# Performance work log

Hardware: AMD Instinct MI355X
Metric: run time of the kernel (lower is better)

## Reference

```python
import jax, jax.numpy as jnp
from jax import lax
import numpy as np

B, CIN, COUT, N, H, W = 16, 64, 64, 8, 128, 128


def setup_inputs() -> dict:
    key = jax.random.key(0)
    ks = jax.random.split(key, 6)
    s = 0.05
    return {
        "x": jax.random.normal(ks[0], (B, CIN, H, W), dtype=jnp.float32),
        "condition": jax.random.normal(ks[1], (B, CIN), dtype=jnp.float32),
        "filt_w": jax.random.normal(ks[2], (N, COUT, CIN, 3, 3), dtype=jnp.float32) * s,
        "filt_b": jax.random.normal(ks[3], (N, COUT), dtype=jnp.float32) * s,
        "sel_w": jax.random.normal(ks[4], (N, CIN), dtype=jnp.float32) * s,
        "sel_b": jax.random.normal(ks[5], (N,), dtype=jnp.float32) * s,
    }


def reference(x, condition, filt_w, filt_b, sel_w, sel_b):
    b = x.shape[0]
    # condition selector: Linear(in_channels -> num_conditions) + softmax
    logits = condition.reshape(b, -1) @ sel_w.T + sel_b          # [B, N]
    weights = jax.nn.softmax(logits, axis=-1)                    # [B, N]

    n, cout, cin, kh, kw = filt_w.shape
    # Run all N branch convs in ONE conv by stacking filters on the output-channel axis.
    kern = filt_w.reshape(n * cout, cin, kh, kw)
    y = lax.conv_general_dilated(
        x, kern, window_strides=(1, 1), padding="SAME",
        dimension_numbers=("NCHW", "OIHW", "NCHW"))              # [B, N*COUT, H, W]
    h, w = y.shape[-2], y.shape[-1]
    y = y.reshape(b, n, cout, h, w) + filt_b.reshape(1, n, cout, 1, 1)
    # softmax-gated sum over the N branches
    out = jnp.einsum("bn,bnohw->bohw", weights, y)
    return out
```

## Files before the change

### kernel.cpp

```cpp
#include <hip/hip_runtime.h>
#include <stdint.h>

#define BATCH 16
#define CIN   64
#define COUT  64
#define NBR   8
#define HH    128
#define WW    128


typedef __attribute__((ext_vector_type(8)))  short short8;
typedef __attribute__((ext_vector_type(16))) float f32x16;

__device__ __forceinline__ unsigned short f2bf(float f) {
    union { float f; uint32_t u; } v; v.f = f;
    uint32_t u = v.u;
    return (unsigned short)((u + 0x7FFFu + ((u >> 16) & 1u)) >> 16);
}

__global__ void k_weights(const float* __restrict__ cond,
                          const float* __restrict__ sel_w,
                          const float* __restrict__ sel_b,
                          float* __restrict__ wt) {
    __shared__ float lg[BATCH][NBR];
    int t = threadIdx.x;
    int b = t >> 3, n = t & 7;
    float acc = sel_b[n];
    #pragma unroll
    for (int c = 0; c < CIN; ++c)
        acc += cond[b * CIN + c] * sel_w[n * CIN + c];
    lg[b][n] = acc;
    __syncthreads();
    float m = -1e30f;
    #pragma unroll
    for (int i = 0; i < NBR; ++i) m = fmaxf(m, lg[b][i]);
    float s = 0.f;
    #pragma unroll
    for (int i = 0; i < NBR; ++i) s += __expf(lg[b][i] - m);
    wt[t] = __expf(lg[b][n] - m) / s;
}

__global__ void k_combine(const float* __restrict__ filt_w,
                          const float* __restrict__ filt_b,
                          const float* __restrict__ wt,
                          unsigned short* __restrict__ wfilt,
                          float* __restrict__ cbias) {
    const int NF = BATCH * 9 * COUT * CIN;
    int idx = blockIdx.x * 256 + threadIdx.x;
    if (idx < NF) {
        int c  = idx & 63;
        int o  = (idx >> 6) & 63;
        int bt = idx >> 12;
        int t  = bt % 9;
        int b  = bt / 9;
        float acc = 0.f;
        #pragma unroll
        for (int n = 0; n < NBR; ++n)
            acc += wt[b * NBR + n] * filt_w[((n * COUT + o) * CIN + c) * 9 + t];
        wfilt[idx] = f2bf(acc);
    } else {
        int j = idx - NF;
        if (j < BATCH * COUT) {
            int b = j >> 6, o = j & 63;
            float acc = 0.f;
            #pragma unroll
            for (int n = 0; n < NBR; ++n)
                acc += wt[b * NBR + n] * filt_b[n * COUT + o];
            cbias[j] = acc;
        }
    }
}

#define RT 8
#define WT 32
#define SLABW 34
#define SLABR 10
#define PSTR  68

__device__ __forceinline__ short8 lds_frag(const unsigned short* p) {
    union { uint2 u[2]; short8 s; } t;
    t.u[0] = *(const uint2*)p;
    t.u[1] = *(const uint2*)(p + 4);
    return t.s;
}
__device__ __forceinline__ short8 gld_frag(const unsigned short* p) {
    union { uint4 u; short8 s; } t;
    t.u = *(const uint4*)p;
    return t.s;
}

__global__ __launch_bounds__(256)
void k_conv(const float* __restrict__ x,
            const unsigned short* __restrict__ wfilt,
            const float* __restrict__ cbias,
            float* __restrict__ out) {
    __shared__ unsigned short lx[SLABR * SLABW * PSTR];
    __shared__ float lbias[COUT];

    const int b  = blockIdx.z;
    const int h0 = blockIdx.y * RT;
    const int w0 = blockIdx.x * WT;
    const int tid = threadIdx.x;

    if (tid < COUT) lbias[tid] = cbias[b * COUT + tid];

    const int NTASK = SLABR * SLABW * 8;
    for (int task = tid; task < NTASK; task += 256) {
        int wc  = task % SLABW;
        int pos = task / SLABW;
        int s   = pos % SLABR;
        int cg  = pos / SLABR;
        int hin = h0 + s - 1;
        int win = w0 + wc - 1;
        unsigned short v[8];
        if (hin >= 0 && hin < HH && win >= 0 && win < WW) {
            const float* px = x + (((long)(b * CIN + cg * 8) * HH + hin) * WW + win);
            #pragma unroll
            for (int j = 0; j < 8; ++j) v[j] = f2bf(px[(long)j * HH * WW]);
        } else {
            #pragma unroll
            for (int j = 0; j < 8; ++j) v[j] = 0;
        }
        int base = (s * SLABW + wc) * PSTR + cg * 8;
        uint2 lo, hi;
        lo.x = (unsigned)v[0] | ((unsigned)v[1] << 16);
        lo.y = (unsigned)v[2] | ((unsigned)v[3] << 16);
        hi.x = (unsigned)v[4] | ((unsigned)v[5] << 16);
        hi.y = (unsigned)v[6] | ((unsigned)v[7] << 16);
        *(uint2*)&lx[base]     = lo;
        *(uint2*)&lx[base + 4] = hi;
    }
    __syncthreads();

    const int lane = tid & 63;
    const int wave = tid >> 6;
    const int l31  = lane & 31;
    const int lh   = lane >> 5;
    const int r0   = wave * 2;

    f32x16 acc00, acc01, acc10, acc11;
    #pragma unroll
    for (int i = 0; i < 16; ++i) { acc00[i] = 0.f; acc01[i] = 0.f; acc10[i] = 0.f; acc11[i] = 0.f; }

    const unsigned short* wf = wfilt + (long)b * 9 * COUT * CIN;

    #pragma unroll
    for (int tap = 0; tap < 9; ++tap) {
        const int kh = tap / 3, kw = tap % 3;
        const unsigned short* wft = wf + (long)tap * COUT * CIN;
        #pragma unroll
        for (int cc = 0; cc < 4; ++cc) {
            const int kofs = cc * 16 + lh * 8;
            short8 a0 = gld_frag(wft + (l31)      * CIN + kofs);
            short8 a1 = gld_frag(wft + (32 + l31) * CIN + kofs);
            short8 b0 = lds_frag(&lx[((r0     + kh) * SLABW + l31 + kw) * PSTR + kofs]);
            short8 b1 = lds_frag(&lx[((r0 + 1 + kh) * SLABW + l31 + kw) * PSTR + kofs]);
            acc00 = __builtin_amdgcn_mfma_f32_32x32x16_bf16(a0, b0, acc00, 0, 0, 0);
            acc01 = __builtin_amdgcn_mfma_f32_32x32x16_bf16(a0, b1, acc01, 0, 0, 0);
            acc10 = __builtin_amdgcn_mfma_f32_32x32x16_bf16(a1, b0, acc10, 0, 0, 0);
            acc11 = __builtin_amdgcn_mfma_f32_32x32x16_bf16(a1, b1, acc11, 0, 0, 0);
        }
    }

    #pragma unroll
    for (int cb = 0; cb < 2; ++cb) {
        #pragma unroll
        for (int pb = 0; pb < 2; ++pb) {
            const f32x16 v = cb == 0 ? (pb == 0 ? acc00 : acc01)
                                     : (pb == 0 ? acc10 : acc11);
            const int hrow = h0 + r0 + pb;
            float* op = out + (((long)(b * COUT + cb * 32) * HH + hrow) * WW + w0 + l31);
            #pragma unroll
            for (int i = 0; i < 16; ++i) {
                int m = (i & 3) + 8 * (i >> 2) + 4 * lh;
                op[(long)m * HH * WW] = v[i] + lbias[cb * 32 + m];
            }
        }
    }
}

extern "C" void kernel_launch(void* const* d_in, const int* in_sizes, int n_in,
                              void* d_out, int out_size, void* d_ws, size_t ws_size,
                              hipStream_t stream) {
    const float* x      = (const float*)d_in[0];
    const float* cond   = (const float*)d_in[1];
    const float* filt_w = (const float*)d_in[2];
    const float* filt_b = (const float*)d_in[3];
    const float* sel_w  = (const float*)d_in[4];
    const float* sel_b  = (const float*)d_in[5];
    float* out = (float*)d_out;

    float* wt             = (float*)d_ws;
    float* cbias          = (float*)((char*)d_ws + 512);
    unsigned short* wfilt = (unsigned short*)((char*)d_ws + 4608);

    k_weights<<<1, 128, 0, stream>>>(cond, sel_w, sel_b, wt);

    const int NF = BATCH * 9 * COUT * CIN + BATCH * COUT;
    k_combine<<<(NF + 255) / 256, 256, 0, stream>>>(filt_w, filt_b, wt, wfilt, cbias);

    dim3 grid(WW / WT, HH / RT, BATCH);
    k_conv<<<grid, 256, 0, stream>>>(x, wfilt, cbias, out);
}
```

Baseline: 196.4 us.

## Fuse softmax and filter combine into one prep kernel; vectorize conv input staging

Merges the softmax-weights and filter-combine kernels into one launch, with each thread computing the softmax locally and combining all 9 taps from contiguous filter reads. The conv kernel now stages input with float4 loads over two channels at a time and uses a cheaper round-to-nearest bf16 conversion. It also seeds the accumulators with the bias instead of adding it at the end, and sets a 3-blocks-per-SM launch bound. The aim is fewer launches, coalesced global loads for the input slab, and less epilogue work. The trade-offs are redundant per-thread logit and softmax work in the prep kernel and a slightly different bf16 rounding on ties.

```diff
diff --git a/kernel.cpp b/kernel.cpp
--- a/kernel.cpp
+++ b/kernel.cpp
@@ -8,66 +8,86 @@
 #define HH    128
 #define WW    128
 
-
 typedef __attribute__((ext_vector_type(8)))  short short8;
 typedef __attribute__((ext_vector_type(16))) float f32x16;
 
+__device__ __forceinline__ unsigned int f2bf_hi(float f) {
+    union { float f; uint32_t u; } v; v.f = f;
+    return (v.u + 0x8000u) >> 16;
+}
 __device__ __forceinline__ unsigned short f2bf(float f) {
     union { float f; uint32_t u; } v; v.f = f;
     uint32_t u = v.u;
     return (unsigned short)((u + 0x7FFFu + ((u >> 16) & 1u)) >> 16);
 }
-
-__global__ void k_weights(const float* __restrict__ cond,
-                          const float* __restrict__ sel_w,
-                          const float* __restrict__ sel_b,
-                          float* __restrict__ wt) {
+__device__ __forceinline__ short8 gld_frag(const unsigned short* p) {
+    union { uint4 u; short8 s; } t;
+    t.u = *(const uint4*)p;
+    return t.s;
+}
+__device__ __forceinline__ short8 lds_frag(const unsigned short* p) {
+    union { uint2 u[2]; short8 s; } t;
+    t.u[0] = *(const uint2*)p;
+    t.u[1] = *(const uint2*)(p + 4);
+    return t.s;
+}
+
+__global__ __launch_bounds__(256)
+void k_prep(const float* __restrict__ cond,
+            const float* __restrict__ sel_w,
+            const float* __restrict__ sel_b,
+            const float* __restrict__ filt_w,
+            const float* __restrict__ filt_b,
+            unsigned short* __restrict__ wfilt,
+            float* __restrict__ cbias) {
     __shared__ float lg[BATCH][NBR];
-    int t = threadIdx.x;
-    int b = t >> 3, n = t & 7;
-    float acc = sel_b[n];
-    #pragma unroll
-    for (int c = 0; c < CIN; ++c)
-        acc += cond[b * CIN + c] * sel_w[n * CIN + c];
-    lg[b][n] = acc;
+    const int tid = threadIdx.x;
+    if (tid < BATCH * NBR) {
+        int b2 = tid >> 3, n = tid & 7;
+        float acc = sel_b[n];
+        #pragma unroll
+        for (int c = 0; c < CIN; ++c)
+            acc += cond[b2 * CIN + c] * sel_w[n * CIN + c];
+        lg[b2][n] = acc;
+    }
     __syncthreads();
-    float m = -1e30f;
-    #pragma unroll
-    for (int i = 0; i < NBR; ++i) m = fmaxf(m, lg[b][i]);
-    float s = 0.f;
-    #pragma unroll
-    for (int i = 0; i < NBR; ++i) s += __expf(lg[b][i] - m);
-    wt[t] = __expf(lg[b][n] - m) / s;
-}
-
-__global__ void k_combine(const float* __restrict__ filt_w,
-                          const float* __restrict__ filt_b,
-                          const float* __restrict__ wt,
-                          unsigned short* __restrict__ wfilt,
-                          float* __restrict__ cbias) {
-    const int NF = BATCH * 9 * COUT * CIN;
-    int idx = blockIdx.x * 256 + threadIdx.x;
-    if (idx < NF) {
-        int c  = idx & 63;
-        int o  = (idx >> 6) & 63;
-        int bt = idx >> 12;
-        int t  = bt % 9;
-        int b  = bt / 9;
-        float acc = 0.f;
-        #pragma unroll
-        for (int n = 0; n < NBR; ++n)
-            acc += wt[b * NBR + n] * filt_w[((n * COUT + o) * CIN + c) * 9 + t];
-        wfilt[idx] = f2bf(acc);
-    } else {
-        int j = idx - NF;
-        if (j < BATCH * COUT) {
-            int b = j >> 6, o = j & 63;
-            float acc = 0.f;
-            #pragma unroll
-            for (int n = 0; n < NBR; ++n)
-                acc += wt[b * NBR + n] * filt_b[n * COUT + o];
-            cbias[j] = acc;
-        }
+
+    const int idx = blockIdx.x * 256 + tid;
+    const int b  = idx >> 12;
+    const int oc = idx & 4095;
+    const int o  = oc >> 6, c = oc & 63;
+
+    float w8[NBR];
+    {
+        float m = -1e30f;
+        #pragma unroll
+        for (int n = 0; n < NBR; ++n) m = fmaxf(m, lg[b][n]);
+        float s = 0.f;
+        #pragma unroll
+        for (int n = 0; n < NBR; ++n) { w8[n] = __expf(lg[b][n] - m); s += w8[n]; }
+        float inv = 1.f / s;
+        #pragma unroll
+        for (int n = 0; n < NBR; ++n) w8[n] *= inv;
+    }
+
+    float acc[9];
+    #pragma unroll
+    for (int t = 0; t < 9; ++t) acc[t] = 0.f;
+    #pragma unroll
+    for (int n = 0; n < NBR; ++n) {
+        const float* p = filt_w + ((long)(n * COUT + o) * CIN + c) * 9;
+        #pragma unroll
+        for (int t = 0; t < 9; ++t) acc[t] += w8[n] * p[t];
+    }
+    #pragma unroll
+    for (int t = 0; t < 9; ++t)
+        wfilt[((long)(b * 9 + t) * 4096) + oc] = f2bf(acc[t]);
+
+    if (oc < COUT) {
+        float ab = 0.f;
+        #pragma unroll
+        for (int n = 0; n < NBR; ++n) ab += w8[n] * filt_b[n * COUT + oc];
+        cbias[b * COUT + oc] = ab;
     }
 }
 
@@ -77,60 +97,46 @@
 #define SLABR 10
 #define PSTR  68
 
-__device__ __forceinline__ short8 lds_frag(const unsigned short* p) {
-    union { uint2 u[2]; short8 s; } t;
-    t.u[0] = *(const uint2*)p;
-    t.u[1] = *(const uint2*)(p + 4);
-    return t.s;
-}
-__device__ __forceinline__ short8 gld_frag(const unsigned short* p) {
-    union { uint4 u; short8 s; } t;
-    t.u = *(const uint4*)p;
-    return t.s;
-}
-
-__global__ __launch_bounds__(256)
-void k_conv(const float* __restrict__ x,
-            const unsigned short* __restrict__ wfilt,
-            const float* __restrict__ cbias,
-            float* __restrict__ out) {
+__global__ __launch_bounds__(256, 3)
+void k_conv3(const float* __restrict__ x,
+             const unsigned short* __restrict__ wfilt,
+             const float* __restrict__ cbias,
+             float* __restrict__ out) {
     __shared__ unsigned short lx[SLABR * SLABW * PSTR];
-    __shared__ float lbias[COUT];
 
     const int b  = blockIdx.z;
     const int h0 = blockIdx.y * RT;
     const int w0 = blockIdx.x * WT;
     const int tid = threadIdx.x;
 
-    if (tid < COUT) lbias[tid] = cbias[b * COUT + tid];
-
-    const int NTASK = SLABR * SLABW * 8;
-    for (int task = tid; task < NTASK; task += 256) {
-        int wc  = task % SLABW;
-        int pos = task / SLABW;
-        int s   = pos % SLABR;
-        int cg  = pos / SLABR;
-        int hin = h0 + s - 1;
-        int win = w0 + wc - 1;
-        unsigned short v[8];
-        if (hin >= 0 && hin < HH && win >= 0 && win < WW) {
-            const float* px = x + (((long)(b * CIN + cg * 8) * HH + hin) * WW + win);
-            #pragma unroll
-            for (int j = 0; j < 8; ++j) v[j] = f2bf(px[(long)j * HH * WW]);
-        } else {
-            #pragma unroll
-            for (int j = 0; j < 8; ++j) v[j] = 0;
-        }
-        int base = (s * SLABW + wc) * PSTR + cg * 8;
-        uint2 lo, hi;
-        lo.x = (unsigned)v[0] | ((unsigned)v[1] << 16);
-        lo.y = (unsigned)v[2] | ((unsigned)v[3] << 16);
-        hi.x = (unsigned)v[4] | ((unsigned)v[5] << 16);
-        hi.y = (unsigned)v[6] | ((unsigned)v[7] << 16);
-        *(uint2*)&lx[base]     = lo;
-        *(uint2*)&lx[base + 4] = hi;
-    }
-    __syncthreads();
+    for (int task = tid; task < SLABR * 32 * 10; task += 256) {
+        const int j  = task % 10;
+        const int r  = task / 10;
+        const int cp = r & 31;
+        const int s  = r >> 5;
+        const int c  = cp * 2;
+        const int hin   = h0 + s - 1;
+        const int wbase = w0 - 4 + j * 4;
+        float4 v0, v1;
+        v0.x = v0.y = v0.z = v0.w = 0.f;
+        v1 = v0;
+        if (hin >= 0 && hin < HH && wbase >= 0 && wbase < WW) {
+            const float* px = x + (((long)(b * CIN + c) * HH + hin) * WW + wbase);
+            v0 = *(const float4*)px;
+            v1 = *(const float4*)(px + (long)HH * WW);
+        }
+        unsigned int d[4];
+        d[0] = f2bf_hi(v0.x) | (f2bf_hi(v1.x) << 16);
+        d[1] = f2bf_hi(v0.y) | (f2bf_hi(v1.y) << 16);
+        d[2] = f2bf_hi(v0.z) | (f2bf_hi(v1.z) << 16);
+        d[3] = f2bf_hi(v0.w) | (f2bf_hi(v1.w) << 16);
+        #pragma unroll
+        for (int i = 0; i < 4; ++i) {
+            const int p = j * 4 - 3 + i;
+            if (p >= 0 && p < SLABW)
+                *(unsigned int*)&lx[(s * SLABW + p) * PSTR + c] = d[i];
+        }
+    }
 
     const int lane = tid & 63;
     const int wave = tid >> 6;
@@ -140,7 +146,15 @@
 
     f32x16 acc00, acc01, acc10, acc11;
     #pragma unroll
-    for (int i = 0; i < 16; ++i) { acc00[i] = 0.f; acc01[i] = 0.f; acc10[i] = 0.f; acc11[i] = 0.f; }
+    for (int i = 0; i < 16; ++i) {
+        const int m = (i & 3) + 8 * (i >> 2) + 4 * lh;
+        const float b0 = cbias[b * COUT + m];
+        const float b1 = cbias[b * COUT + 32 + m];
+        acc00[i] = b0; acc01[i] = b0;
+        acc10[i] = b1; acc11[i] = b1;
+    }
+
+    __syncthreads();
 
     const unsigned short* wf = wfilt + (long)b * 9 * COUT * CIN;
 
@@ -151,7 +165,7 @@
         #pragma unroll
         for (int cc = 0; cc < 4; ++cc) {
             const int kofs = cc * 16 + lh * 8;
-            short8 a0 = gld_frag(wft + (l31)      * CIN + kofs);
+            short8 a0 = gld_frag(wft + l31 * CIN + kofs);
             short8 a1 = gld_frag(wft + (32 + l31) * CIN + kofs);
             short8 b0 = lds_frag(&lx[((r0     + kh) * SLABW + l31 + kw) * PSTR + kofs]);
             short8 b1 = lds_frag(&lx[((r0 + 1 + kh) * SLABW + l31 + kw) * PSTR + kofs]);
@@ -172,8 +186,8 @@
             float* op = out + (((long)(b * COUT + cb * 32) * HH + hrow) * WW + w0 + l31);
             #pragma unroll
             for (int i = 0; i < 16; ++i) {
-                int m = (i & 3) + 8 * (i >> 2) + 4 * lh;
-                op[(long)m * HH * WW] = v[i] + lbias[cb * 32 + m];
+                const int m = (i & 3) + 8 * (i >> 2) + 4 * lh;
+                op[(long)m * HH * WW] = v[i];
             }
         }
     }
@@ -190,15 +204,11 @@
     const float* sel_b  = (const float*)d_in[5];
     float* out = (float*)d_out;
 
-    float* wt             = (float*)d_ws;
-    float* cbias          = (float*)((char*)d_ws + 512);
-    unsigned short* wfilt = (unsigned short*)((char*)d_ws + 4608);
-
-    k_weights<<<1, 128, 0, stream>>>(cond, sel_w, sel_b, wt);
-
-    const int NF = BATCH * 9 * COUT * CIN + BATCH * COUT;
-    k_combine<<<(NF + 255) / 256, 256, 0, stream>>>(filt_w, filt_b, wt, wfilt, cbias);
+    float*          cbias = (float*)d_ws;
+    unsigned short* wfilt = (unsigned short*)((char*)d_ws + 4096);
+
+    k_prep<<<256, 256, 0, stream>>>(cond, sel_w, sel_b, filt_w, filt_b, wfilt, cbias);
 
     dim3 grid(WW / WT, HH / RT, BATCH);
-    k_conv<<<grid, 256, 0, stream>>>(x, wfilt, cbias, out);
-}
+    k_conv3<<<grid, 256, 0, stream>>>(x, wfilt, cbias, out);
+}
```

Result: faster. 192.2 us (-2.1%).
